# Kernel optimization log

Measured on AMD Instinct MI355X. Metric: run time of the kernel, lower is better.

The kernel has to match this reference:

```python
import jax, jax.numpy as jnp
import numpy as np

N_NODES = 50000
N_EDGES = 800000
NUM_GRAPHS = 4
IN_DIM, HID_DIM, OUT_DIM = 1024, 128, 1
MAX_RISK = 5.0


def gcn_conv(x, W, b, src, dst, n):
    """PyG GCNConv: add self-loops, sym-normalize, gather-GEMM-scatter."""
    loop = jnp.arange(n, dtype=src.dtype)
    s = jnp.concatenate([src, loop])
    d = jnp.concatenate([dst, loop])
    deg = jax.ops.segment_sum(jnp.ones_like(d, dtype=x.dtype), d, num_segments=n)
    dinv = jnp.where(deg > 0, jax.lax.rsqrt(deg), 0.0)
    norm = dinv[s] * dinv[d]  # [E+N]
    xw = x @ W                # dense GEMM first (fewer FLOPs than per-edge)
    msg = xw[s] * norm[:, None]          # irregular gather, [E+N, out]
    out = jax.ops.segment_sum(msg, d, num_segments=n)  # scatter-add
    return out + b


def setup_inputs() -> dict:
    key = jax.random.key(0)
    ks = jax.random.split(key, 12)
    x = jax.random.normal(ks[0], (N_NODES, IN_DIM), dtype=jnp.float32)
    edge_index = jax.random.randint(ks[1], (2, N_EDGES), 0, N_NODES, dtype=jnp.int64)
    batch = jnp.sort(jax.random.randint(ks[2], (N_NODES,), 0, NUM_GRAPHS, dtype=jnp.int64))

    def glorot(k, fan_in, fan_out):
        s = np.sqrt(6.0 / (fan_in + fan_out)).astype(np.float32)
        return jax.random.uniform(k, (fan_in, fan_out), jnp.float32, -s, s)

    params = {
        'W0': glorot(ks[3], IN_DIM, HID_DIM),  'b0': jnp.zeros((HID_DIM,), jnp.float32),
        'W1': glorot(ks[4], HID_DIM, HID_DIM), 'b1': jnp.zeros((HID_DIM,), jnp.float32),
        'W2': glorot(ks[5], HID_DIM, HID_DIM), 'b2': jnp.zeros((HID_DIM,), jnp.float32),
        'Wl1': glorot(ks[6], 2 * HID_DIM, HID_DIM), 'bl1': jnp.zeros((HID_DIM,), jnp.float32),
        'Wl2': glorot(ks[7], HID_DIM, HID_DIM // 2), 'bl2': jnp.zeros((HID_DIM // 2,), jnp.float32),
        'Wl3': glorot(ks[8], HID_DIM // 2, OUT_DIM), 'bl3': jnp.zeros((OUT_DIM,), jnp.float32),
    }
    return dict(x=x, edge_index=edge_index, batch=batch, **params)


def reference(x, edge_index, batch, W0, b0, W1, b1, W2, b2, Wl1, bl1, Wl2, bl2, Wl3, bl3):
    n = x.shape[0]
    src, dst = edge_index[0], edge_index[1]
    h = jax.nn.relu(gcn_conv(x, W0, b0, src, dst, n))
    h = jax.nn.relu(gcn_conv(h, W1, b1, src, dst, n))
    h = jax.nn.relu(gcn_conv(h, W2, b2, src, dst, n))
    # global max pool + global mean pool per graph
    gmax = jax.ops.segment_max(h, batch, num_segments=NUM_GRAPHS)
    gsum = jax.ops.segment_sum(h, batch, num_segments=NUM_GRAPHS)
    cnt = jax.ops.segment_sum(jnp.ones((n,), h.dtype), batch, num_segments=NUM_GRAPHS)
    gmean = gsum / jnp.maximum(cnt, 1.0)[:, None]
    g = jnp.concatenate([gmax, gmean], axis=1)  # [G, 2*hid]
    g = jax.nn.relu(g @ Wl1 + bl1)
    g = jax.nn.relu(g @ Wl2 + bl2)
    out = g @ Wl3 + bl3
    return jnp.minimum(out, MAX_RISK)
```

## Files before the change

kernel.cpp:

```cpp
#include <hip/hip_runtime.h>
#include <math.h>

#define HID 128
#define NGRAPH 4

typedef int idx_t;
typedef short bf16x8 __attribute__((ext_vector_type(8)));
typedef float f32x4 __attribute__((ext_vector_type(4)));
typedef _Float16 f16x8 __attribute__((ext_vector_type(8)));
typedef unsigned short u16x8 __attribute__((ext_vector_type(8)));

__device__ inline ushort f2bf(float f) {
  uint u = __float_as_uint(f);
  u += 0x7FFF + ((u >> 16) & 1);
  return (ushort)(u >> 16);
}
__device__ inline float bf2f(ushort h) { return __uint_as_float(((uint)h) << 16); }

__device__ inline int sw(int row, int slot) {
  return (row << 5) + ((slot ^ ((row >> 1) & 3)) << 3);
}

__global__ __launch_bounds__(256) void k_count(const idx_t* __restrict__ dst,
                                               int* __restrict__ cnt, int E) {
  int e = blockIdx.x * 256 + threadIdx.x;
  if (e < E) atomicAdd(&cnt[dst[e]], 1);
}

#define SC 1024
__global__ __launch_bounds__(256) void k_scan1(const int* __restrict__ cnt,
                                               int* __restrict__ bsum, int n) {
  __shared__ int sh[256];
  int base = blockIdx.x * SC + threadIdx.x * 4;
  int s = 0;
#pragma unroll
  for (int j = 0; j < 4; ++j) { int i = base + j; if (i < n) s += cnt[i]; }
  sh[threadIdx.x] = s;
  __syncthreads();
  for (int o = 128; o > 0; o >>= 1) {
    if (threadIdx.x < o) sh[threadIdx.x] += sh[threadIdx.x + o];
    __syncthreads();
  }
  if (threadIdx.x == 0) bsum[blockIdx.x] = sh[0];
}

__global__ __launch_bounds__(64) void k_scan2(const int* __restrict__ bsum,
                                              int* __restrict__ boff,
                                              int* __restrict__ off, int nb, int n) {
  int lane = threadIdx.x;
  int v = (lane < nb) ? bsum[lane] : 0;
  for (int d = 1; d < 64; d <<= 1) {
    int t = __shfl_up(v, d);
    if (lane >= d) v += t;
  }
  int ex = __shfl_up(v, 1);
  if (lane == 0) ex = 0;
  if (lane < nb) boff[lane] = ex;
  if (lane == nb - 1) off[n] = v;
}

__global__ __launch_bounds__(256) void k_scan3(const int* __restrict__ cnt,
                                               const int* __restrict__ boff,
                                               int* __restrict__ off,
                                               float* __restrict__ dinv, int n) {
  __shared__ int sh[256];
  int base = blockIdx.x * SC + threadIdx.x * 4;
  int c[4];
  int s = 0;
#pragma unroll
  for (int j = 0; j < 4; ++j) {
    int i = base + j;
    c[j] = (i < n) ? cnt[i] : 0;
    s += c[j];
  }
  sh[threadIdx.x] = s;
  __syncthreads();
  for (int o = 1; o < 256; o <<= 1) {
    int t = (threadIdx.x >= (unsigned)o) ? sh[threadIdx.x - o] : 0;
    __syncthreads();
    sh[threadIdx.x] += t;
    __syncthreads();
  }
  int ex = sh[threadIdx.x] - s + boff[blockIdx.x];
#pragma unroll
  for (int j = 0; j < 4; ++j) {
    int i = base + j;
    if (i < n) {
      off[i] = ex;
      dinv[i] = 1.0f / sqrtf((float)c[j] + 1.0f);
      ex += c[j];
    }
  }
}

__global__ __launch_bounds__(256) void k_fill(const idx_t* __restrict__ src,
                                              const idx_t* __restrict__ dst,
                                              const int* __restrict__ off,
                                              const float* __restrict__ dinv,
                                              int* __restrict__ fillc,
                                              int2* __restrict__ edata, int E) {
  int e = blockIdx.x * 256 + threadIdx.x;
  if (e < E) {
    int s = src[e], d = dst[e];
    int p = atomicAdd(&fillc[d], 1);
    float w = dinv[s] * dinv[d];
    edata[off[d] + p] = make_int2(s, __float_as_int(w));
  }
}

__global__ __launch_bounds__(256) void k_wsplit(const float* __restrict__ W,
                                                ushort* __restrict__ Wh,
                                                ushort* __restrict__ Wl, int K) {
  int i = blockIdx.x * 256 + threadIdx.x;
  if (i >= K * HID) return;
  int k = i >> 7, n = i & 127;
  float f = W[i];
  ushort h = f2bf(f);
  Wh[(size_t)n * K + k] = h;
  Wl[(size_t)n * K + k] = f2bf(f - bf2f(h));
}

template <int K>
__global__ __launch_bounds__(256) void k_gemm2(const float* __restrict__ X,
                                               const ushort* __restrict__ Wh,
                                               const ushort* __restrict__ Wl,
                                               _Float16* __restrict__ Y16, int M) {
  __shared__ __align__(16) ushort BhL[2][128 * 32];
  __shared__ __align__(16) ushort BlL[2][128 * 32];
  const int tid = threadIdx.x;
  const int wid = tid >> 6, lane = tid & 63;
  const int lrow = lane & 15, kg = lane >> 4;
  const int row0 = blockIdx.x * 128;
  const int r0 = row0 + wid * 32 + lrow;
  const int r1 = r0 + 16;
  const bool ok0 = r0 < M, ok1 = r1 < M;
  const float* xp0 = X + (size_t)(ok0 ? r0 : 0) * K + kg * 8;
  const float* xp1 = X + (size_t)(ok1 ? r1 : 0) * K + kg * 8;
  const int c0 = tid >> 2, s0 = tid & 3;
  const int c1 = (tid + 256) >> 2, s1 = tid & 3;
  const ushort* wh0 = Wh + (size_t)c0 * K + s0 * 8;
  const ushort* wh1 = Wh + (size_t)c1 * K + s1 * 8;
  const ushort* wl0 = Wl + (size_t)c0 * K + s0 * 8;
  const ushort* wl1 = Wl + (size_t)c1 * K + s1 * 8;
  const int d0 = sw(c0, s0), d1 = sw(c1, s1);

  f32x4 acc[2][8] = {};
  float4 aA0, aA1, aA2, aA3, aB0, aB1, aB2, aB3;
  u16x8 bA0, bA1, bA2, bA3, bB0, bB1, bB2, bB3;

#define LOAD_A(k0, a0, a1, a2, a3)                                        \
  {                                                                       \
    a0 = ok0 ? *(const float4*)(xp0 + (k0)) : make_float4(0, 0, 0, 0);    \
    a1 = ok0 ? *(const float4*)(xp0 + (k0) + 4) : make_float4(0, 0, 0, 0);\
    a2 = ok1 ? *(const float4*)(xp1 + (k0)) : make_float4(0, 0, 0, 0);    \
    a3 = ok1 ? *(const float4*)(xp1 + (k0) + 4) : make_float4(0, 0, 0, 0);\
  }
#define LOAD_B(k0, b0, b1, b2, b3)                                        \
  {                                                                       \
    b0 = *(const u16x8*)(wh0 + (k0)); b1 = *(const u16x8*)(wh1 + (k0));   \
    b2 = *(const u16x8*)(wl0 + (k0)); b3 = *(const u16x8*)(wl1 + (k0));   \
  }
#define WRITE_B(buf, b0, b1, b2, b3)                                      \
  {                                                                       \
    *(u16x8*)&BhL[buf][d0] = b0; *(u16x8*)&BhL[buf][d1] = b1;             \
    *(u16x8*)&BlL[buf][d0] = b2; *(u16x8*)&BlL[buf][d1] = b3;             \
  }
#define CONV8(v0, v1, hdst, ldst)                                         \
  {                                                                       \
    float tf[8] = {v0.x, v0.y, v0.z, v0.w, v1.x, v1.y, v1.z, v1.w};       \
    _Pragma("unroll")                                                     \
    for (int j = 0; j < 8; ++j) {                                         \
      ushort hb = f2bf(tf[j]);                                            \
      hdst[j] = (short)hb;                                                \
      ldst[j] = (short)f2bf(tf[j] - bf2f(hb));                            \
    }                                                                     \
  }
#define MFMA_STEP(buf, ah0, al0, ah1, al1)                                \
  {                                                                       \
    _Pragma("unroll")                                                     \
    for (int ni = 0; ni < 8; ++ni) {                                      \
      int c = ni * 16 + lrow;                                             \
      bf16x8 bh = *(const bf16x8*)&BhL[buf][sw(c, kg)];                   \
      bf16x8 bl = *(const bf16x8*)&BlL[buf][sw(c, kg)];                   \
      acc[0][ni] = __builtin_amdgcn_mfma_f32_16x16x32_bf16(ah0, bh, acc[0][ni], 0, 0, 0); \
      acc[0][ni] = __builtin_amdgcn_mfma_f32_16x16x32_bf16(al0, bh, acc[0][ni], 0, 0, 0); \
      acc[0][ni] = __builtin_amdgcn_mfma_f32_16x16x32_bf16(ah0, bl, acc[0][ni], 0, 0, 0); \
      acc[1][ni] = __builtin_amdgcn_mfma_f32_16x16x32_bf16(ah1, bh, acc[1][ni], 0, 0, 0); \
      acc[1][ni] = __builtin_amdgcn_mfma_f32_16x16x32_bf16(al1, bh, acc[1][ni], 0, 0, 0); \
      acc[1][ni] = __builtin_amdgcn_mfma_f32_16x16x32_bf16(ah1, bl, acc[1][ni], 0, 0, 0); \
    }                                                                     \
  }

  LOAD_A(0, aA0, aA1, aA2, aA3);
  LOAD_B(0, bA0, bA1, bA2, bA3);
  WRITE_B(0, bA0, bA1, bA2, bA3);
  if (K > 32) {
    LOAD_A(32, aB0, aB1, aB2, aB3);
    LOAD_B(32, bB0, bB1, bB2, bB3);
  }
  __syncthreads();

  for (int k0 = 0; k0 < K; k0 += 64) {
    {
      if (k0 + 32 < K) WRITE_B(1, bB0, bB1, bB2, bB3);
      bf16x8 ah0, al0, ah1, al1;
      CONV8(aA0, aA1, ah0, al0);
      CONV8(aA2, aA3, ah1, al1);
      if (k0 + 64 < K) {
        LOAD_A(k0 + 64, aA0, aA1, aA2, aA3);
        LOAD_B(k0 + 64, bA0, bA1, bA2, bA3);
      }
      MFMA_STEP(0, ah0, al0, ah1, al1);
      __syncthreads();
    }
    if (k0 + 32 >= K) break;
    {
      if (k0 + 96 < K) WRITE_B(0, bA0, bA1, bA2, bA3);
      bf16x8 ah0, al0, ah1, al1;
      CONV8(aB0, aB1, ah0, al0);
      CONV8(aB2, aB3, ah1, al1);
      if (k0 + 96 < K) {
        LOAD_A(k0 + 96, aB0, aB1, aB2, aB3);
        LOAD_B(k0 + 96, bB0, bB1, bB2, bB3);
      }
      MFMA_STEP(1, ah0, al0, ah1, al1);
      __syncthreads();
    }
  }
#pragma unroll
  for (int mi = 0; mi < 2; ++mi)
#pragma unroll
    for (int ni = 0; ni < 8; ++ni)
#pragma unroll
      for (int r = 0; r < 4; ++r) {
        int grow = row0 + wid * 32 + mi * 16 + kg * 4 + r;
        if (grow < M)
          Y16[(size_t)grow * HID + ni * 16 + lrow] = (_Float16)acc[mi][ni][r];
      }
#undef LOAD_A
#undef LOAD_B
#undef WRITE_B
#undef CONV8
#undef MFMA_STEP
}

__global__ __launch_bounds__(256) void k_agg16(const _Float16* __restrict__ xh,
                                               const float* __restrict__ dinv,
                                               const int* __restrict__ off,
                                               const int2* __restrict__ edata,
                                               const float* __restrict__ bias,
                                               float* __restrict__ hout, int n) {
  int v = blockIdx.x * 4 + (threadIdx.x >> 6);
  if (v >= n) return;
  int lane = threadIdx.x & 63;
  int grp = lane >> 4, gl = lane & 15;
  int fb = gl * 8;
  float acc[8] = {0.f, 0.f, 0.f, 0.f, 0.f, 0.f, 0.f, 0.f};
  int j0 = off[v], j1 = off[v + 1];
  for (int j = j0 + grp; j < j1; j += 4) {
    int2 e = edata[j];
    float w = __int_as_float(e.y);
    f16x8 m = *(const f16x8*)&xh[(size_t)e.x * HID + fb];
#pragma unroll
    for (int q = 0; q < 8; ++q) acc[q] = fmaf(w, (float)m[q], acc[q]);
  }
#pragma unroll
  for (int q = 0; q < 8; ++q) {
    acc[q] += __shfl_xor(acc[q], 16);
    acc[q] += __shfl_xor(acc[q], 32);
  }
  if (grp == 0) {
    float dv = dinv[v], dv2 = dv * dv;
    f16x8 sv = *(const f16x8*)&xh[(size_t)v * HID + fb];
    const float4 b0 = *(const float4*)&bias[fb];
    const float4 b1 = *(const float4*)&bias[fb + 4];
    float4 o0, o1;
    o0.x = fmaxf(fmaf(dv2, (float)sv[0], acc[0]) + b0.x, 0.f);
    o0.y = fmaxf(fmaf(dv2, (float)sv[1], acc[1]) + b0.y, 0.f);
    o0.z = fmaxf(fmaf(dv2, (float)sv[2], acc[2]) + b0.z, 0.f);
    o0.w = fmaxf(fmaf(dv2, (float)sv[3], acc[3]) + b0.w, 0.f);
    o1.x = fmaxf(fmaf(dv2, (float)sv[4], acc[4]) + b1.x, 0.f);
    o1.y = fmaxf(fmaf(dv2, (float)sv[5], acc[5]) + b1.y, 0.f);
    o1.z = fmaxf(fmaf(dv2, (float)sv[6], acc[6]) + b1.z, 0.f);
    o1.w = fmaxf(fmaf(dv2, (float)sv[7], acc[7]) + b1.w, 0.f);
    *(float4*)&hout[(size_t)v * HID + fb] = o0;
    *(float4*)&hout[(size_t)v * HID + fb + 4] = o1;
  }
}

__global__ __launch_bounds__(256) void k_gcnt(const idx_t* __restrict__ batch,
                                              int* __restrict__ gcnt, int n) {
  __shared__ int h[NGRAPH];
  int tid = threadIdx.x;
  if (tid < NGRAPH) h[tid] = 0;
  __syncthreads();
  int i = blockIdx.x * 256 + tid;
  if (i < n) atomicAdd(&h[batch[i]], 1);
  __syncthreads();
  if (tid < NGRAPH && h[tid]) atomicAdd(&gcnt[tid], h[tid]);
}

__global__ __launch_bounds__(128) void k_pool(const float* __restrict__ h,
                                              const idx_t* __restrict__ batch,
                                              float* __restrict__ gmax,
                                              float* __restrict__ gsum, int n) {
  int f = threadIdx.x;
  int v0 = blockIdx.x * 128;
  int cur = -1;
  float mx = 0.f, sm = 0.f;
  for (int i = 0; i < 128; ++i) {
    int v = v0 + i;
    if (v >= n) break;
    int g = batch[v];
    if (g != cur) {
      if (cur >= 0) {
        atomicMax((int*)&gmax[cur * HID + f], __float_as_int(mx));
        atomicAdd(&gsum[cur * HID + f], sm);
      }
      cur = g; mx = 0.f; sm = 0.f;
    }
    float val = h[(size_t)v * HID + f];
    mx = fmaxf(mx, val);
    sm += val;
  }
  if (cur >= 0) {
    atomicMax((int*)&gmax[cur * HID + f], __float_as_int(mx));
    atomicAdd(&gsum[cur * HID + f], sm);
  }
}

__global__ __launch_bounds__(256) void k_mlp(const float* __restrict__ gmax,
                                             const float* __restrict__ gsum,
                                             const int* __restrict__ gcnt,
                                             const float* __restrict__ Wl1,
                                             const float* __restrict__ bl1,
                                             const float* __restrict__ Wl2,
                                             const float* __restrict__ bl2,
                                             const float* __restrict__ Wl3,
                                             const float* __restrict__ bl3,
                                             float* __restrict__ out) {
  __shared__ float G[NGRAPH][2 * HID];
  __shared__ float H1[NGRAPH][HID];
  __shared__ float H2[NGRAPH][HID / 2];
  int t = threadIdx.x;
  for (int i = t; i < NGRAPH * 2 * HID; i += 256) {
    int gi = i >> 8, j = i & 255;
    float val;
    if (j < HID) val = gmax[gi * HID + j];
    else val = gsum[gi * HID + (j - HID)] / fmaxf((float)gcnt[gi], 1.0f);
    G[gi][j] = val;
  }
  __syncthreads();
  for (int i = t; i < NGRAPH * HID; i += 256) {
    int gi = i >> 7, j = i & 127;
    float a = bl1[j];
    for (int k = 0; k < 2 * HID; ++k) a = fmaf(G[gi][k], Wl1[k * HID + j], a);
    H1[gi][j] = fmaxf(a, 0.f);
  }
  __syncthreads();
  {
    int gi = t >> 6, j = t & 63;
    float a = bl2[j];
    for (int k = 0; k < HID; ++k) a = fmaf(H1[gi][k], Wl2[k * 64 + j], a);
    H2[gi][j] = fmaxf(a, 0.f);
  }
  __syncthreads();
  if (t < NGRAPH) {
    float a = bl3[0];
    for (int k = 0; k < 64; ++k) a = fmaf(H2[t][k], Wl3[k], a);
    out[t] = fminf(a, 5.0f);
  }
}

extern "C" void kernel_launch(void* const* d_in, const int* in_sizes, int n_in,
                              void* d_out, int out_size, void* d_ws, size_t ws_size,
                              hipStream_t stream) {
  const float* x   = (const float*)d_in[0];
  const idx_t* ei  = (const idx_t*)d_in[1];
  const idx_t* bat = (const idx_t*)d_in[2];
  const float* W0 = (const float*)d_in[3];  const float* b0 = (const float*)d_in[4];
  const float* W1 = (const float*)d_in[5];  const float* b1 = (const float*)d_in[6];
  const float* W2 = (const float*)d_in[7];  const float* b2 = (const float*)d_in[8];
  const float* Wl1 = (const float*)d_in[9];  const float* bl1 = (const float*)d_in[10];
  const float* Wl2 = (const float*)d_in[11]; const float* bl2 = (const float*)d_in[12];
  const float* Wl3 = (const float*)d_in[13]; const float* bl3 = (const float*)d_in[14];
  float* out = (float*)d_out;

  const int N = in_sizes[2];
  const int E = in_sizes[1] / 2;
  const idx_t* srcv = ei;
  const idx_t* dstv = ei + E;
  const int nb = (N + SC - 1) / SC;

  char* ws = (char*)d_ws;
  size_t o = 0;
  auto alloc = [&](size_t bytes) -> void* {
    void* p = ws + o;
    o = (o + bytes + 255) & ~(size_t)255;
    return p;
  };
  _Float16* xh   = (_Float16*)alloc((size_t)N * HID * 2);
  float* bufB    = (float*)alloc((size_t)N * HID * 4);
  float* dinv = (float*)alloc((size_t)N * 4);
  int* cnt    = (int*)alloc((size_t)N * 4);
  int* off    = (int*)alloc((size_t)(N + 1) * 4);
  int* fillc  = (int*)alloc((size_t)N * 4);
  int2* edata = (int2*)alloc((size_t)E * 8);
  int* bsum   = (int*)alloc(64 * 4);
  int* boff   = (int*)alloc(64 * 4);
  ushort* Wh0 = (ushort*)alloc((size_t)1024 * HID * 2);
  ushort* Wl0 = (ushort*)alloc((size_t)1024 * HID * 2);
  ushort* Wh1 = (ushort*)alloc((size_t)HID * HID * 2);
  ushort* Wlo1 = (ushort*)alloc((size_t)HID * HID * 2);
  ushort* Wh2 = (ushort*)alloc((size_t)HID * HID * 2);
  ushort* Wlo2 = (ushort*)alloc((size_t)HID * HID * 2);
  float* gmax = (float*)alloc(NGRAPH * HID * 4);
  float* gsum = (float*)alloc(NGRAPH * HID * 4);
  int* gcnt   = (int*)alloc(NGRAPH * 4);

  hipMemsetAsync(cnt, 0, (size_t)N * 4, stream);
  hipMemsetAsync(fillc, 0, (size_t)N * 4, stream);
  hipMemsetAsync(gmax, 0, NGRAPH * HID * 4, stream);
  hipMemsetAsync(gsum, 0, NGRAPH * HID * 4, stream);
  hipMemsetAsync(gcnt, 0, NGRAPH * 4, stream);

  k_wsplit<<<(1024 * HID + 255) / 256, 256, 0, stream>>>(W0, Wh0, Wl0, 1024);
  k_wsplit<<<(HID * HID + 255) / 256, 256, 0, stream>>>(W1, Wh1, Wlo1, HID);
  k_wsplit<<<(HID * HID + 255) / 256, 256, 0, stream>>>(W2, Wh2, Wlo2, HID);

  k_count<<<(E + 255) / 256, 256, 0, stream>>>(dstv, cnt, E);
  k_scan1<<<nb, 256, 0, stream>>>(cnt, bsum, N);
  k_scan2<<<1, 64, 0, stream>>>(bsum, boff, off, nb, N);
  k_scan3<<<nb, 256, 0, stream>>>(cnt, boff, off, dinv, N);
  k_fill<<<(E + 255) / 256, 256, 0, stream>>>(srcv, dstv, off, dinv, fillc, edata, E);

  const int gblk = (N + 127) / 128;
  const int ablk = (N + 3) / 4;
  k_gemm2<1024><<<gblk, 256, 0, stream>>>(x, Wh0, Wl0, xh, N);
  k_agg16<<<ablk, 256, 0, stream>>>(xh, dinv, off, edata, b0, bufB, N);
  k_gemm2<HID><<<gblk, 256, 0, stream>>>(bufB, Wh1, Wlo1, xh, N);
  k_agg16<<<ablk, 256, 0, stream>>>(xh, dinv, off, edata, b1, bufB, N);
  k_gemm2<HID><<<gblk, 256, 0, stream>>>(bufB, Wh2, Wlo2, xh, N);
  k_agg16<<<ablk, 256, 0, stream>>>(xh, dinv, off, edata, b2, bufB, N);

  k_gcnt<<<(N + 255) / 256, 256, 0, stream>>>(bat, gcnt, N);
  k_pool<<<(N + 127) / 128, 128, 0, stream>>>(bufB, bat, gmax, gsum, N);
  k_mlp<<<1, 256, 0, stream>>>(gmax, gsum, gcnt, Wl1, bl1, Wl2, bl2, Wl3, bl3, out);
}
```

Baseline: 391.7 us.

## Switch GEMMs to fp16 split MFMA, store hidden activations as fp16

The split-precision GEMM now uses fp16 hi/lo pieces with f16 MFMAs instead of bf16. Hidden-layer activations are stored in fp16, so layers 2 and 3 read half the bytes and skip the A-operand split, doing two MFMAs per tile instead of three. Block tiles shrink from 128 to 64 rows, and the aggregation kernel handles 16 features per lane across 8 edge groups. The intent is to cut GEMM compute and activation memory traffic. In exchange, fp16 has less range than bf16 and the intermediate activations carry fp16 rounding.

```diff
diff --git a/kernel.cpp b/kernel.cpp
--- a/kernel.cpp
+++ b/kernel.cpp
@@ -5,17 +5,8 @@
 #define NGRAPH 4
 
 typedef int idx_t;
-typedef short bf16x8 __attribute__((ext_vector_type(8)));
 typedef float f32x4 __attribute__((ext_vector_type(4)));
-typedef _Float16 f16x8 __attribute__((ext_vector_type(8)));
-typedef unsigned short u16x8 __attribute__((ext_vector_type(8)));
-
-__device__ inline ushort f2bf(float f) {
-  uint u = __float_as_uint(f);
-  u += 0x7FFF + ((u >> 16) & 1);
-  return (ushort)(u >> 16);
-}
-__device__ inline float bf2f(ushort h) { return __uint_as_float(((uint)h) << 16); }
+typedef _Float16 h8 __attribute__((ext_vector_type(8)));
 
 __device__ inline int sw(int row, int slot) {
   return (row << 5) + ((slot ^ ((row >> 1) & 3)) << 3);
@@ -109,93 +100,85 @@
 }
 
 __global__ __launch_bounds__(256) void k_wsplit(const float* __restrict__ W,
-                                                ushort* __restrict__ Wh,
-                                                ushort* __restrict__ Wl, int K) {
+                                                _Float16* __restrict__ Wh,
+                                                _Float16* __restrict__ Wl, int K) {
   int i = blockIdx.x * 256 + threadIdx.x;
   if (i >= K * HID) return;
   int k = i >> 7, n = i & 127;
   float f = W[i];
-  ushort h = f2bf(f);
+  _Float16 h = (_Float16)f;
   Wh[(size_t)n * K + k] = h;
-  Wl[(size_t)n * K + k] = f2bf(f - bf2f(h));
-}
-
-template <int K>
-__global__ __launch_bounds__(256) void k_gemm2(const float* __restrict__ X,
-                                               const ushort* __restrict__ Wh,
-                                               const ushort* __restrict__ Wl,
+  Wl[(size_t)n * K + k] = (_Float16)(f - (float)h);
+}
+
+template <int K, bool F32>
+__global__ __launch_bounds__(256) void k_gemm3(const void* __restrict__ Xv,
+                                               const _Float16* __restrict__ Wh,
+                                               const _Float16* __restrict__ Wl,
                                                _Float16* __restrict__ Y16, int M) {
-  __shared__ __align__(16) ushort BhL[2][128 * 32];
-  __shared__ __align__(16) ushort BlL[2][128 * 32];
+  __shared__ __align__(16) _Float16 BhL[2][128 * 32];
+  __shared__ __align__(16) _Float16 BlL[2][128 * 32];
   const int tid = threadIdx.x;
   const int wid = tid >> 6, lane = tid & 63;
   const int lrow = lane & 15, kg = lane >> 4;
-  const int row0 = blockIdx.x * 128;
-  const int r0 = row0 + wid * 32 + lrow;
-  const int r1 = r0 + 16;
-  const bool ok0 = r0 < M, ok1 = r1 < M;
-  const float* xp0 = X + (size_t)(ok0 ? r0 : 0) * K + kg * 8;
-  const float* xp1 = X + (size_t)(ok1 ? r1 : 0) * K + kg * 8;
+  const int row0 = blockIdx.x * 64;
+  const int r = row0 + wid * 16 + lrow;
+  const int rc = (r < M) ? r : 0;
+  const float* xf = (const float*)Xv + (size_t)rc * K + kg * 8;
+  const _Float16* xg = (const _Float16*)Xv + (size_t)rc * K + kg * 8;
   const int c0 = tid >> 2, s0 = tid & 3;
-  const int c1 = (tid + 256) >> 2, s1 = tid & 3;
-  const ushort* wh0 = Wh + (size_t)c0 * K + s0 * 8;
-  const ushort* wh1 = Wh + (size_t)c1 * K + s1 * 8;
-  const ushort* wl0 = Wl + (size_t)c0 * K + s0 * 8;
-  const ushort* wl1 = Wl + (size_t)c1 * K + s1 * 8;
-  const int d0 = sw(c0, s0), d1 = sw(c1, s1);
-
-  f32x4 acc[2][8] = {};
-  float4 aA0, aA1, aA2, aA3, aB0, aB1, aB2, aB3;
-  u16x8 bA0, bA1, bA2, bA3, bB0, bB1, bB2, bB3;
-
-#define LOAD_A(k0, a0, a1, a2, a3)                                        \
-  {                                                                       \
-    a0 = ok0 ? *(const float4*)(xp0 + (k0)) : make_float4(0, 0, 0, 0);    \
-    a1 = ok0 ? *(const float4*)(xp0 + (k0) + 4) : make_float4(0, 0, 0, 0);\
-    a2 = ok1 ? *(const float4*)(xp1 + (k0)) : make_float4(0, 0, 0, 0);    \
-    a3 = ok1 ? *(const float4*)(xp1 + (k0) + 4) : make_float4(0, 0, 0, 0);\
-  }
+  const int c1 = 64 + c0;
+  const _Float16* wh0 = Wh + (size_t)c0 * K + s0 * 8;
+  const _Float16* wh1 = Wh + (size_t)c1 * K + s0 * 8;
+  const _Float16* wl0 = Wl + (size_t)c0 * K + s0 * 8;
+  const _Float16* wl1 = Wl + (size_t)c1 * K + s0 * 8;
+  const int d0 = sw(c0, s0), d1 = sw(c1, s0);
+
+  f32x4 acc[8] = {};
+  float4 aA0, aA1, aB0, aB1;
+  h8 gA, gB;
+  h8 bA0, bA1, bA2, bA3, bB0, bB1, bB2, bB3;
+
+#define LOAD_A0(k0)                                                       \
+  { if (F32) { aA0 = *(const float4*)(xf + (k0));                         \
+               aA1 = *(const float4*)(xf + (k0) + 4); }                   \
+    else gA = *(const h8*)(xg + (k0)); }
+#define LOAD_A1(k0)                                                       \
+  { if (F32) { aB0 = *(const float4*)(xf + (k0));                         \
+               aB1 = *(const float4*)(xf + (k0) + 4); }                   \
+    else gB = *(const h8*)(xg + (k0)); }
 #define LOAD_B(k0, b0, b1, b2, b3)                                        \
-  {                                                                       \
-    b0 = *(const u16x8*)(wh0 + (k0)); b1 = *(const u16x8*)(wh1 + (k0));   \
-    b2 = *(const u16x8*)(wl0 + (k0)); b3 = *(const u16x8*)(wl1 + (k0));   \
-  }
+  { b0 = *(const h8*)(wh0 + (k0)); b1 = *(const h8*)(wh1 + (k0));         \
+    b2 = *(const h8*)(wl0 + (k0)); b3 = *(const h8*)(wl1 + (k0)); }
 #define WRITE_B(buf, b0, b1, b2, b3)                                      \
-  {                                                                       \
-    *(u16x8*)&BhL[buf][d0] = b0; *(u16x8*)&BhL[buf][d1] = b1;             \
-    *(u16x8*)&BlL[buf][d0] = b2; *(u16x8*)&BlL[buf][d1] = b3;             \
-  }
-#define CONV8(v0, v1, hdst, ldst)                                         \
-  {                                                                       \
-    float tf[8] = {v0.x, v0.y, v0.z, v0.w, v1.x, v1.y, v1.z, v1.w};       \
-    _Pragma("unroll")                                                     \
-    for (int j = 0; j < 8; ++j) {                                         \
-      ushort hb = f2bf(tf[j]);                                            \
-      hdst[j] = (short)hb;                                                \
-      ldst[j] = (short)f2bf(tf[j] - bf2f(hb));                            \
-    }                                                                     \
-  }
-#define MFMA_STEP(buf, ah0, al0, ah1, al1)                                \
-  {                                                                       \
-    _Pragma("unroll")                                                     \
+  { *(h8*)&BhL[buf][d0] = b0; *(h8*)&BhL[buf][d1] = b1;                   \
+    *(h8*)&BlL[buf][d0] = b2; *(h8*)&BlL[buf][d1] = b3; }
+#define CONV(v0, v1, g, ah, al)                                           \
+  { if (F32) {                                                            \
+      float tf[8] = {v0.x, v0.y, v0.z, v0.w, v1.x, v1.y, v1.z, v1.w};     \
+      _Pragma("unroll")                                                   \
+      for (int j = 0; j < 8; ++j) {                                       \
+        _Float16 hh = (_Float16)tf[j];                                    \
+        ah[j] = hh; al[j] = (_Float16)(tf[j] - (float)hh);                \
+      }                                                                   \
+    } else ah = g; }
+#define MFMA_STEP(buf, ah, al)                                            \
+  { _Pragma("unroll")                                                     \
     for (int ni = 0; ni < 8; ++ni) {                                      \
       int c = ni * 16 + lrow;                                             \
-      bf16x8 bh = *(const bf16x8*)&BhL[buf][sw(c, kg)];                   \
-      bf16x8 bl = *(const bf16x8*)&BlL[buf][sw(c, kg)];                   \
-      acc[0][ni] = __builtin_amdgcn_mfma_f32_16x16x32_bf16(ah0, bh, acc[0][ni], 0, 0, 0); \
-      acc[0][ni] = __builtin_amdgcn_mfma_f32_16x16x32_bf16(al0, bh, acc[0][ni], 0, 0, 0); \
-      acc[0][ni] = __builtin_amdgcn_mfma_f32_16x16x32_bf16(ah0, bl, acc[0][ni], 0, 0, 0); \
-      acc[1][ni] = __builtin_amdgcn_mfma_f32_16x16x32_bf16(ah1, bh, acc[1][ni], 0, 0, 0); \
-      acc[1][ni] = __builtin_amdgcn_mfma_f32_16x16x32_bf16(al1, bh, acc[1][ni], 0, 0, 0); \
-      acc[1][ni] = __builtin_amdgcn_mfma_f32_16x16x32_bf16(ah1, bl, acc[1][ni], 0, 0, 0); \
-    }                                                                     \
-  }
-
-  LOAD_A(0, aA0, aA1, aA2, aA3);
+      h8 bh = *(const h8*)&BhL[buf][sw(c, kg)];                           \
+      h8 bl = *(const h8*)&BlL[buf][sw(c, kg)];                           \
+      acc[ni] = __builtin_amdgcn_mfma_f32_16x16x32_f16(ah, bh, acc[ni], 0, 0, 0); \
+      if (F32)                                                            \
+        acc[ni] = __builtin_amdgcn_mfma_f32_16x16x32_f16(al, bh, acc[ni], 0, 0, 0); \
+      acc[ni] = __builtin_amdgcn_mfma_f32_16x16x32_f16(ah, bl, acc[ni], 0, 0, 0); \
+    } }
+
+  LOAD_A0(0);
   LOAD_B(0, bA0, bA1, bA2, bA3);
   WRITE_B(0, bA0, bA1, bA2, bA3);
   if (K > 32) {
-    LOAD_A(32, aB0, aB1, aB2, aB3);
+    LOAD_A1(32);
     LOAD_B(32, bB0, bB1, bB2, bB3);
   }
   __syncthreads();
@@ -203,44 +186,41 @@
   for (int k0 = 0; k0 < K; k0 += 64) {
     {
       if (k0 + 32 < K) WRITE_B(1, bB0, bB1, bB2, bB3);
-      bf16x8 ah0, al0, ah1, al1;
-      CONV8(aA0, aA1, ah0, al0);
-      CONV8(aA2, aA3, ah1, al1);
+      h8 ah, al;
+      CONV(aA0, aA1, gA, ah, al);
       if (k0 + 64 < K) {
-        LOAD_A(k0 + 64, aA0, aA1, aA2, aA3);
+        LOAD_A0(k0 + 64);
         LOAD_B(k0 + 64, bA0, bA1, bA2, bA3);
       }
-      MFMA_STEP(0, ah0, al0, ah1, al1);
+      MFMA_STEP(0, ah, al);
       __syncthreads();
     }
     if (k0 + 32 >= K) break;
     {
       if (k0 + 96 < K) WRITE_B(0, bA0, bA1, bA2, bA3);
-      bf16x8 ah0, al0, ah1, al1;
-      CONV8(aB0, aB1, ah0, al0);
-      CONV8(aB2, aB3, ah1, al1);
+      h8 ah, al;
+      CONV(aB0, aB1, gB, ah, al);
       if (k0 + 96 < K) {
-        LOAD_A(k0 + 96, aB0, aB1, aB2, aB3);
+        LOAD_A1(k0 + 96);
         LOAD_B(k0 + 96, bB0, bB1, bB2, bB3);
       }
-      MFMA_STEP(1, ah0, al0, ah1, al1);
+      MFMA_STEP(1, ah, al);
       __syncthreads();
     }
   }
 #pragma unroll
-  for (int mi = 0; mi < 2; ++mi)
-#pragma unroll
-    for (int ni = 0; ni < 8; ++ni)
-#pragma unroll
-      for (int r = 0; r < 4; ++r) {
-        int grow = row0 + wid * 32 + mi * 16 + kg * 4 + r;
-        if (grow < M)
-          Y16[(size_t)grow * HID + ni * 16 + lrow] = (_Float16)acc[mi][ni][r];
-      }
-#undef LOAD_A
+  for (int ni = 0; ni < 8; ++ni)
+#pragma unroll
+    for (int rr = 0; rr < 4; ++rr) {
+      int grow = row0 + wid * 16 + kg * 4 + rr;
+      if (grow < M)
+        Y16[(size_t)grow * HID + ni * 16 + lrow] = (_Float16)acc[ni][rr];
+    }
+#undef LOAD_A0
+#undef LOAD_A1
 #undef LOAD_B
 #undef WRITE_B
-#undef CONV8
+#undef CONV
 #undef MFMA_STEP
 }
 
@@ -249,42 +229,46 @@
                                                const int* __restrict__ off,
                                                const int2* __restrict__ edata,
                                                const float* __restrict__ bias,
-                                               float* __restrict__ hout, int n) {
+                                               _Float16* __restrict__ hout, int n) {
   int v = blockIdx.x * 4 + (threadIdx.x >> 6);
   if (v >= n) return;
   int lane = threadIdx.x & 63;
-  int grp = lane >> 4, gl = lane & 15;
-  int fb = gl * 8;
-  float acc[8] = {0.f, 0.f, 0.f, 0.f, 0.f, 0.f, 0.f, 0.f};
+  int grp = lane >> 3, gl = lane & 7;
+  int fb = gl * 16;
+  float acc[16] = {0.f, 0.f, 0.f, 0.f, 0.f, 0.f, 0.f, 0.f,
+                   0.f, 0.f, 0.f, 0.f, 0.f, 0.f, 0.f, 0.f};
   int j0 = off[v], j1 = off[v + 1];
-  for (int j = j0 + grp; j < j1; j += 4) {
+  for (int j = j0 + grp; j < j1; j += 8) {
     int2 e = edata[j];
     float w = __int_as_float(e.y);
-    f16x8 m = *(const f16x8*)&xh[(size_t)e.x * HID + fb];
-#pragma unroll
-    for (int q = 0; q < 8; ++q) acc[q] = fmaf(w, (float)m[q], acc[q]);
-  }
-#pragma unroll
-  for (int q = 0; q < 8; ++q) {
+    h8 m0 = *(const h8*)&xh[(size_t)e.x * HID + fb];
+    h8 m1 = *(const h8*)&xh[(size_t)e.x * HID + fb + 8];
+#pragma unroll
+    for (int q = 0; q < 8; ++q) {
+      acc[q] = fmaf(w, (float)m0[q], acc[q]);
+      acc[8 + q] = fmaf(w, (float)m1[q], acc[8 + q]);
+    }
+  }
+#pragma unroll
+  for (int q = 0; q < 16; ++q) {
+    acc[q] += __shfl_xor(acc[q], 8);
     acc[q] += __shfl_xor(acc[q], 16);
     acc[q] += __shfl_xor(acc[q], 32);
   }
   if (grp == 0) {
     float dv = dinv[v], dv2 = dv * dv;
-    f16x8 sv = *(const f16x8*)&xh[(size_t)v * HID + fb];
-    const float4 b0 = *(const float4*)&bias[fb];
-    const float4 b1 = *(const float4*)&bias[fb + 4];
-    float4 o0, o1;
-    o0.x = fmaxf(fmaf(dv2, (float)sv[0], acc[0]) + b0.x, 0.f);
-    o0.y = fmaxf(fmaf(dv2, (float)sv[1], acc[1]) + b0.y, 0.f);
-    o0.z = fmaxf(fmaf(dv2, (float)sv[2], acc[2]) + b0.z, 0.f);
-    o0.w = fmaxf(fmaf(dv2, (float)sv[3], acc[3]) + b0.w, 0.f);
-    o1.x = fmaxf(fmaf(dv2, (float)sv[4], acc[4]) + b1.x, 0.f);
-    o1.y = fmaxf(fmaf(dv2, (float)sv[5], acc[5]) + b1.y, 0.f);
-    o1.z = fmaxf(fmaf(dv2, (float)sv[6], acc[6]) + b1.z, 0.f);
-    o1.w = fmaxf(fmaf(dv2, (float)sv[7], acc[7]) + b1.w, 0.f);
-    *(float4*)&hout[(size_t)v * HID + fb] = o0;
-    *(float4*)&hout[(size_t)v * HID + fb + 4] = o1;
+    h8 s0 = *(const h8*)&xh[(size_t)v * HID + fb];
+    h8 s1 = *(const h8*)&xh[(size_t)v * HID + fb + 8];
+    h8 o0, o1;
+#pragma unroll
+    for (int q = 0; q < 8; ++q) {
+      float a0 = fmaxf(fmaf(dv2, (float)s0[q], acc[q]) + bias[fb + q], 0.f);
+      float a1 = fmaxf(fmaf(dv2, (float)s1[q], acc[8 + q]) + bias[fb + 8 + q], 0.f);
+      o0[q] = (_Float16)a0;
+      o1[q] = (_Float16)a1;
+    }
+    *(h8*)&hout[(size_t)v * HID + fb] = o0;
+    *(h8*)&hout[(size_t)v * HID + fb + 8] = o1;
   }
 }
 
@@ -300,7 +284,7 @@
   if (tid < NGRAPH && h[tid]) atomicAdd(&gcnt[tid], h[tid]);
 }
 
-__global__ __launch_bounds__(128) void k_pool(const float* __restrict__ h,
+__global__ __launch_bounds__(128) void k_pool(const _Float16* __restrict__ h,
                                               const idx_t* __restrict__ batch,
                                               float* __restrict__ gmax,
                                               float* __restrict__ gsum, int n) {
@@ -319,7 +303,7 @@
       }
       cur = g; mx = 0.f; sm = 0.f;
     }
-    float val = h[(size_t)v * HID + f];
+    float val = (float)h[(size_t)v * HID + f];
     mx = fmaxf(mx, val);
     sm += val;
   }
@@ -399,8 +383,8 @@
     o = (o + bytes + 255) & ~(size_t)255;
     return p;
   };
-  _Float16* xh   = (_Float16*)alloc((size_t)N * HID * 2);
-  float* bufB    = (float*)alloc((size_t)N * HID * 4);
+  _Float16* xh  = (_Float16*)alloc((size_t)N * HID * 2);
+  _Float16* h16 = (_Float16*)alloc((size_t)N * HID * 2);
   float* dinv = (float*)alloc((size_t)N * 4);
   int* cnt    = (int*)alloc((size_t)N * 4);
   int* off    = (int*)alloc((size_t)(N + 1) * 4);
@@ -408,12 +392,12 @@
   int2* edata = (int2*)alloc((size_t)E * 8);
   int* bsum   = (int*)alloc(64 * 4);
   int* boff   = (int*)alloc(64 * 4);
-  ushort* Wh0 = (ushort*)alloc((size_t)1024 * HID * 2);
-  ushort* Wl0 = (ushort*)alloc((size_t)1024 * HID * 2);
-  ushort* Wh1 = (ushort*)alloc((size_t)HID * HID * 2);
-  ushort* Wlo1 = (ushort*)alloc((size_t)HID * HID * 2);
-  ushort* Wh2 = (ushort*)alloc((size_t)HID * HID * 2);
-  ushort* Wlo2 = (ushort*)alloc((size_t)HID * HID * 2);
+  _Float16* Wh0 = (_Float16*)alloc((size_t)1024 * HID * 2);
+  _Float16* Wl0 = (_Float16*)alloc((size_t)1024 * HID * 2);
+  _Float16* Wh1 = (_Float16*)alloc((size_t)HID * HID * 2);
+  _Float16* Wlo1 = (_Float16*)alloc((size_t)HID * HID * 2);
+  _Float16* Wh2 = (_Float16*)alloc((size_t)HID * HID * 2);
+  _Float16* Wlo2 = (_Float16*)alloc((size_t)HID * HID * 2);
   float* gmax = (float*)alloc(NGRAPH * HID * 4);
   float* gsum = (float*)alloc(NGRAPH * HID * 4);
   int* gcnt   = (int*)alloc(NGRAPH * 4);
@@ -434,16 +418,16 @@
   k_scan3<<<nb, 256, 0, stream>>>(cnt, boff, off, dinv, N);
   k_fill<<<(E + 255) / 256, 256, 0, stream>>>(srcv, dstv, off, dinv, fillc, edata, E);
 
-  const int gblk = (N + 127) / 128;
+  const int gblk = (N + 63) / 64;
   const int ablk = (N + 3) / 4;
-  k_gemm2<1024><<<gblk, 256, 0, stream>>>(x, Wh0, Wl0, xh, N);
-  k_agg16<<<ablk, 256, 0, stream>>>(xh, dinv, off, edata, b0, bufB, N);
-  k_gemm2<HID><<<gblk, 256, 0, stream>>>(bufB, Wh1, Wlo1, xh, N);
-  k_agg16<<<ablk, 256, 0, stream>>>(xh, dinv, off, edata, b1, bufB, N);
-  k_gemm2<HID><<<gblk, 256, 0, stream>>>(bufB, Wh2, Wlo2, xh, N);
-  k_agg16<<<ablk, 256, 0, stream>>>(xh, dinv, off, edata, b2, bufB, N);
+  k_gemm3<1024, true><<<gblk, 256, 0, stream>>>(x, Wh0, Wl0, xh, N);
+  k_agg16<<<ablk, 256, 0, stream>>>(xh, dinv, off, edata, b0, h16, N);
+  k_gemm3<HID, false><<<gblk, 256, 0, stream>>>(h16, Wh1, Wlo1, xh, N);
+  k_agg16<<<ablk, 256, 0, stream>>>(xh, dinv, off, edata, b1, h16, N);
+  k_gemm3<HID, false><<<gblk, 256, 0, stream>>>(h16, Wh2, Wlo2, xh, N);
+  k_agg16<<<ablk, 256, 0, stream>>>(xh, dinv, off, edata, b2, h16, N);
 
   k_gcnt<<<(N + 255) / 256, 256, 0, stream>>>(bat, gcnt, N);
-  k_pool<<<(N + 127) / 128, 128, 0, stream>>>(bufB, bat, gmax, gsum, N);
+  k_pool<<<(N + 127) / 128, 128, 0, stream>>>(h16, bat, gmax, gsum, N);
   k_mlp<<<1, 256, 0, stream>>>(gmax, gsum, gcnt, Wl1, bl1, Wl2, bl2, Wl3, bl3, out);
 }
```

New measurement: 370.6 us. -5.4%, faster.
